# Performance work log

Measured on AMD Instinct MI355X. Metric: run time of the kernel, lower is better.

## Reference

```python
import jax, jax.numpy as jnp
import numpy as np

B, S, E = 2, 2048, 2048
H, KV, HD = 16, 4, 128  # num_heads, num_kv_heads, head_dim
G = H // KV             # query heads per kv head
ROPE_BASE = 10000.0


def rope_tables(dim, maxlen):
    freqs = 1.0 / ROPE_BASE ** (jnp.arange(0, dim, 2, dtype=jnp.float32) / dim)
    t = jnp.arange(maxlen, dtype=jnp.float32)
    f = jnp.outer(t, freqs)  # (maxlen, dim//2)
    return jnp.cos(f), jnp.sin(f)


def apply_rope(x, cos, sin):
    # x: (..., seq, heads, head_dim); interleaved-pair rotation
    s_len = x.shape[-3]
    c = cos[:s_len][:, None, :]
    s = sin[:s_len][:, None, :]
    x1 = x[..., ::2]
    x2 = x[..., 1::2]
    return jnp.stack([x1 * c - x2 * s, x1 * s + x2 * c], axis=-1).reshape(x.shape)


def setup_inputs() -> dict:
    key = jax.random.key(0)
    kx, kq, kk, kv, ko = jax.random.split(key, 5)
    x = jax.random.normal(kx, (B, S, E), dtype=jnp.float32)
    Wq = jax.random.normal(kq, (E, H * HD), dtype=jnp.float32) * 0.02
    Wk = jax.random.normal(kk, (E, KV * HD), dtype=jnp.float32) * 0.02
    Wv = jax.random.normal(kv, (E, KV * HD), dtype=jnp.float32) * 0.02
    Wo = jax.random.normal(ko, (H * HD, E), dtype=jnp.float32) * 0.02
    mask = jnp.tril(jnp.ones((S, S), dtype=bool))[None, None]  # causal (1,1,S,S)
    return {"x": x, "Wq": Wq, "Wk": Wk, "Wv": Wv, "Wo": Wo, "mask": mask}


def reference(x, Wq, Wk, Wv, Wo, mask):
    b, s, _ = x.shape
    cos, sin = rope_tables(HD, s)
    q = (x @ Wq).reshape(b, s, H, HD)
    k = (x @ Wk).reshape(b, s, KV, HD)
    v = (x @ Wv).reshape(b, s, KV, HD)
    q = apply_rope(q, cos, sin)
    k = apply_rope(k, cos, sin)
    if G > 1:
        k = jnp.repeat(k, G, axis=2)  # (b, s, H, HD)
        v = jnp.repeat(v, G, axis=2)
    q = jnp.transpose(q, (0, 2, 1, 3))  # (b, H, s, HD)
    k = jnp.transpose(k, (0, 2, 1, 3))
    v = jnp.transpose(v, (0, 2, 1, 3))
    scale = jnp.sqrt(jnp.float32(HD)).astype(q.dtype)
    scores = jnp.einsum("bhqd,bhkd->bhqk", q, k) / scale
    scores = jnp.where(mask, scores, jnp.finfo(scores.dtype).min)
    attn = jax.nn.softmax(scores, axis=-1)
    out = jnp.einsum("bhqk,bhkd->bhqd", attn, v)
    out = jnp.transpose(out, (0, 2, 1, 3)).reshape(b, s, H * HD)
    return out @ Wo
```

## Files before the change

kernel.cpp:

```cpp
#include <hip/hip_runtime.h>
#include <hip/hip_bf16.h>
#include <cstdint>

#define B_ 2
#define S_ 2048
#define E_ 2048
#define H_ 16
#define KV_ 4
#define HD_ 128
#define BS_ (B_*S_)
#define QKV_LD 3072
#define SM_SCALE 0.08838834764831845f
#define SC_LOG2E 0.1275424488538497f

typedef __attribute__((ext_vector_type(8))) __bf16 bf16x8;
typedef __attribute__((ext_vector_type(4))) float  floatx4;

__device__ __forceinline__ unsigned short f2bf(float f) {
  union { float f; unsigned u; } v; v.f = f;
  unsigned r = v.u + 0x7fffu + ((v.u >> 16) & 1u);
  return (unsigned short)(r >> 16);
}
__device__ __forceinline__ float bf2f(unsigned short u) {
  union { unsigned u; float f; } v; v.u = ((unsigned)u) << 16; return v.f;
}
__device__ __forceinline__ unsigned pack_bf16x2(float a, float b) {
  union { __hip_bfloat162 h; unsigned u; } v;
  v.h = __float22bfloat162_rn(make_float2(a, b));
  return v.u;
}

__device__ __forceinline__ void async_cp16(const void* g, void* l) {
  __builtin_amdgcn_global_load_lds(
      (const __attribute__((address_space(1))) void*)g,
      (__attribute__((address_space(3))) void*)l, 16, 0, 0);
}

__global__ __launch_bounds__(256)
void cvt_bf16(const float* __restrict__ src, unsigned short* __restrict__ dst,
              int n4) {
  int idx = blockIdx.x * 256 + threadIdx.x;
  if (idx >= n4) return;
  float4 v = *(const float4*)(src + (size_t)idx * 4);
  ushort4 o;
  o.x = f2bf(v.x); o.y = f2bf(v.y); o.z = f2bf(v.z); o.w = f2bf(v.w);
  *(ushort4*)(dst + (size_t)idx * 4) = o;
}

__global__ __launch_bounds__(256)
void cvt_bf16_t(const float* __restrict__ src, unsigned short* __restrict__ dst,
                int N, int dld, int noff) {
  __shared__ float tile[64 * 65];
  const int t = threadIdx.x;
  const int bk = blockIdx.y * 64, bn = blockIdx.x * 64;
  const int r = t >> 2, cg = t & 3;
#pragma unroll
  for (int i = 0; i < 4; ++i) {
    int c = cg * 16 + i * 4;
    float4 v = *(const float4*)(src + (size_t)(bk + r) * N + bn + c);
    tile[r * 65 + c] = v.x; tile[r * 65 + c + 1] = v.y;
    tile[r * 65 + c + 2] = v.z; tile[r * 65 + c + 3] = v.w;
  }
  __syncthreads();
  const int nl = t >> 2, kg = t & 3;
  union { unsigned short u[16]; uint4 q[2]; } o;
#pragma unroll
  for (int j = 0; j < 16; ++j)
    o.u[j] = f2bf(tile[(kg * 16 + j) * 65 + nl]);
  unsigned short* dp = dst + (size_t)(noff + bn + nl) * dld + bk + kg * 16;
  *(uint4*)(dp) = o.q[0];
  *(uint4*)(dp + 8) = o.q[1];
}

__global__ __launch_bounds__(256)
void rope_kernel(unsigned short* __restrict__ qkv) {
  const int PPR = 1280;
  int idx = blockIdx.x * 256 + threadIdx.x;
  if (idx >= BS_ * PPR) return;
  int row = idx / PPR, p = idx - row * PPR;
  int col = (p < 1024) ? (2 * p) : (2048 + 2 * (p - 1024));
  int d = p & 63;
  int s = row & (S_ - 1);
  float freq = expf(-(float)d * 0.14391156831212787f);
  float ang = (float)s * freq;
  float c = cosf(ang), sn = sinf(ang);
  unsigned short* ptr = qkv + (size_t)row * QKV_LD + col;
  float x1 = bf2f(ptr[0]), x2 = bf2f(ptr[1]);
  ptr[0] = f2bf(x1 * c - x2 * sn);
  ptr[1] = f2bf(x1 * sn + x2 * c);
}

__global__ __launch_bounds__(256)
void vtrans_kernel(const unsigned short* __restrict__ qkv,
                   unsigned short* __restrict__ vt) {
  __shared__ unsigned short tile[64 * 72];
  const int tid = threadIdx.x;
  const int s0 = blockIdx.x * 64;
  const int g = blockIdx.y >> 1;
  const int hh = (blockIdx.y & 1) * 64;
  const int b = g >> 2, kvh = g & 3;
#pragma unroll
  for (int i = 0; i < 2; ++i) {
    int chunk = tid + i * 256;
    int r = chunk >> 3, c = (chunk & 7) * 8;
    uint4 v = *(const uint4*)(qkv + (size_t)(b * S_ + s0 + r) * QKV_LD + 2560 + kvh * HD_ + hh + c);
    *(uint4*)(tile + r * 72 + c) = v;
  }
  __syncthreads();
#pragma unroll
  for (int i = 0; i < 2; ++i) {
    int chunk = tid + i * 256;
    int hdr = chunk >> 3, sc = (chunk & 7) * 8;
    union { unsigned short u[8]; uint4 v; } t;
#pragma unroll
    for (int j = 0; j < 8; ++j) t.u[j] = tile[(sc + j) * 72 + hdr];
    *(uint4*)(vt + (size_t)(g * HD_ + hh + hdr) * S_ + s0 + sc) = t.v;
  }
}

template<bool OUT_BF16>
__global__ __launch_bounds__(512, 2)
void gemm8(const unsigned short* __restrict__ A,
           const unsigned short* __restrict__ BT,
           void* __restrict__ C, int M, int N, int K) {
  __shared__ unsigned short Ash[2][256 * 64];
  __shared__ unsigned short Bsh[2][256 * 64];
  const int tid = threadIdx.x, l = tid & 63, w = tid >> 6;
  const int l16 = l & 15, l4 = l >> 4;
  const int w2 = w >> 2, w3 = w & 3;

  const int ntn = (int)gridDim.x;
  const int nwg = (int)(gridDim.x * gridDim.y);
  const int orig = (int)blockIdx.y * ntn + (int)blockIdx.x;
  const int cpx = nwg >> 3;
  const int swz = (orig & 7) * cpx + (orig >> 3);
  const int bm = (swz / ntn) * 256, bn = (swz % ntn) * 256;

  const int srow = tid >> 3;
  const int sgrp = ((tid & 7) - (tid >> 3)) & 7;
  const unsigned short* Asrc = A  + (size_t)(bm + srow) * K + sgrp * 8;
  const unsigned short* Bsrc = BT + (size_t)(bn + srow) * K + sgrp * 8;
  const int ldst = w * 512;

#define STAGE_A8(buf, H, kb) do { \
    async_cp16(Asrc + (size_t)((H) * 128) * K + (kb),      &Ash[buf][(H) * 8192 + ldst]); \
    async_cp16(Asrc + (size_t)((H) * 128 + 64) * K + (kb), &Ash[buf][(H) * 8192 + 4096 + ldst]); \
  } while (0)
#define STAGE_B8(buf, H, kb) do { \
    async_cp16(Bsrc + (size_t)((H) * 128) * K + (kb),      &Bsh[buf][(H) * 8192 + ldst]); \
    async_cp16(Bsrc + (size_t)((H) * 128 + 64) * K + (kb), &Bsh[buf][(H) * 8192 + 4096 + ldst]); \
  } while (0)
#define BAR8() __builtin_amdgcn_s_barrier()
#define VMCNT4() asm volatile("s_waitcnt vmcnt(4)" ::: "memory")

  const int s0 = ((l4 + l16) & 7) * 8;
  const int s1 = ((l4 + l16 + 4) & 7) * 8;
  const int arb = w2 * 64 + l16;
  const int brb = w3 * 32 + l16;

  const int nkt = K >> 6;

  STAGE_B8(0, 0, 0);
  STAGE_A8(0, 1, 0);
  STAGE_A8(0, 0, 0);
  STAGE_B8(0, 1, 0);
  {
    const int kb1 = (nkt > 1) ? 64 : 0;
    STAGE_B8(1, 0, kb1);
    STAGE_A8(1, 1, kb1);
  }
  VMCNT4(); BAR8();

  floatx4 acc[2][4][2][2] = {};

  for (int kt = 0; kt < nkt; ++kt) {
    const int cur = kt & 1;
    const int kb1 = ((kt + 1 < nkt) ? kt + 1 : nkt - 1) << 6;
    const int kb2 = ((kt + 2 < nkt) ? kt + 2 : nkt - 1) << 6;
    bf16x8 a[4][2], b0[2][2], b1[2][2];

#pragma unroll
    for (int m = 0; m < 4; ++m) {
      const int rA = 128 + arb + m * 16;
      a[m][0] = *(const bf16x8*)(&Ash[cur][rA * 64 + s0]);
      a[m][1] = *(const bf16x8*)(&Ash[cur][rA * 64 + s1]);
    }
#pragma unroll
    for (int n = 0; n < 2; ++n) {
      const int rB = brb + n * 16;
      b0[n][0] = *(const bf16x8*)(&Bsh[cur][rB * 64 + s0]);
      b0[n][1] = *(const bf16x8*)(&Bsh[cur][rB * 64 + s1]);
    }
    STAGE_A8(cur ^ 1, 0, kb1);
    BAR8();
    __builtin_amdgcn_s_setprio(1);
#pragma unroll
    for (int m = 0; m < 4; ++m)
#pragma unroll
      for (int n = 0; n < 2; ++n) {
        acc[1][m][0][n] = __builtin_amdgcn_mfma_f32_16x16x32_bf16(a[m][0], b0[n][0], acc[1][m][0][n], 0, 0, 0);
        acc[1][m][0][n] = __builtin_amdgcn_mfma_f32_16x16x32_bf16(a[m][1], b0[n][1], acc[1][m][0][n], 0, 0, 0);
      }
    __builtin_amdgcn_s_setprio(0);
    BAR8();

#pragma unroll
    for (int n = 0; n < 2; ++n) {
      const int rB = 128 + brb + n * 16;
      b1[n][0] = *(const bf16x8*)(&Bsh[cur][rB * 64 + s0]);
      b1[n][1] = *(const bf16x8*)(&Bsh[cur][rB * 64 + s1]);
    }
    STAGE_B8(cur ^ 1, 1, kb1);
    BAR8();
    __builtin_amdgcn_s_setprio(1);
#pragma unroll
    for (int m = 0; m < 4; ++m)
#pragma unroll
      for (int n = 0; n < 2; ++n) {
        acc[1][m][1][n] = __builtin_amdgcn_mfma_f32_16x16x32_bf16(a[m][0], b1[n][0], acc[1][m][1][n], 0, 0, 0);
        acc[1][m][1][n] = __builtin_amdgcn_mfma_f32_16x16x32_bf16(a[m][1], b1[n][1], acc[1][m][1][n], 0, 0, 0);
      }
    __builtin_amdgcn_s_setprio(0);
    BAR8();

#pragma unroll
    for (int m = 0; m < 4; ++m) {
      const int rA = arb + m * 16;
      a[m][0] = *(const bf16x8*)(&Ash[cur][rA * 64 + s0]);
      a[m][1] = *(const bf16x8*)(&Ash[cur][rA * 64 + s1]);
    }
    STAGE_B8(cur, 0, kb2);
    BAR8();
    __builtin_amdgcn_s_setprio(1);
#pragma unroll
    for (int m = 0; m < 4; ++m)
#pragma unroll
      for (int n = 0; n < 2; ++n) {
        acc[0][m][1][n] = __builtin_amdgcn_mfma_f32_16x16x32_bf16(a[m][0], b1[n][0], acc[0][m][1][n], 0, 0, 0);
        acc[0][m][1][n] = __builtin_amdgcn_mfma_f32_16x16x32_bf16(a[m][1], b1[n][1], acc[0][m][1][n], 0, 0, 0);
      }
    __builtin_amdgcn_s_setprio(0);
    BAR8();

    STAGE_A8(cur, 1, kb2);
    BAR8();
    __builtin_amdgcn_s_setprio(1);
#pragma unroll
    for (int m = 0; m < 4; ++m)
#pragma unroll
      for (int n = 0; n < 2; ++n) {
        acc[0][m][0][n] = __builtin_amdgcn_mfma_f32_16x16x32_bf16(a[m][0], b0[n][0], acc[0][m][0][n], 0, 0, 0);
        acc[0][m][0][n] = __builtin_amdgcn_mfma_f32_16x16x32_bf16(a[m][1], b0[n][1], acc[0][m][0][n], 0, 0, 0);
      }
    __builtin_amdgcn_s_setprio(0);
    VMCNT4();
    BAR8();
  }

  asm volatile("s_waitcnt vmcnt(0)" ::: "memory");

#pragma unroll
  for (int mh = 0; mh < 2; ++mh)
#pragma unroll
    for (int m = 0; m < 4; ++m)
#pragma unroll
      for (int nh = 0; nh < 2; ++nh)
#pragma unroll
        for (int n = 0; n < 2; ++n) {
          const int row0 = bm + mh * 128 + w2 * 64 + m * 16 + l4 * 4;
          const int col  = bn + nh * 128 + w3 * 32 + n * 16 + l16;
#pragma unroll
          for (int rr = 0; rr < 4; ++rr) {
            float v = acc[mh][m][nh][n][rr];
            if (OUT_BF16) ((unsigned short*)C)[(size_t)(row0 + rr) * N + col] = f2bf(v);
            else          ((float*)C)[(size_t)(row0 + rr) * N + col] = v;
          }
        }
#undef STAGE_A8
#undef STAGE_B8
#undef BAR8
#undef VMCNT4
}

__global__ __launch_bounds__(512, 2)
void gqa_attention(const unsigned short* __restrict__ qkv,
                   const unsigned short* __restrict__ vt,
                   unsigned short* __restrict__ out) {
  __shared__ unsigned short Ksh[2][2][32 * 128];
  __shared__ unsigned short Vsh[2][2][128 * 32];

  const int tid = threadIdx.x, l = tid & 63, wave = tid >> 6;
  const int l16 = l & 15, l4 = l >> 4;
  const int hw = wave & 3, seg = wave >> 2;
  const int g = blockIdx.x, b = g >> 2, kvh = g & 3;
  const int h = kvh * 4 + hw;
  const int y = blockIdx.y;

  const int k_subrow = l >> 4;
  const int v_subrow = l >> 2;
  const int gv = (((l & 3) - (l >> 4)) & 3) * 8;

  const unsigned short* kp[2];
  const unsigned short* vp[2];
#pragma unroll
  for (int i = 0; i < 2; ++i) {
    int cc = hw + i * 4;
    int krow = 4 * cc + k_subrow;
    int gk = (((l & 15) - krow) & 15) * 8;
    kp[i] = qkv + (size_t)(b * S_ + krow) * QKV_LD + 2048 + kvh * HD_ + gk;
    vp[i] = vt + (size_t)(g * HD_ + 16 * cc + v_subrow) * S_ + gv;
  }

  for (int phase = 0; phase < 2; ++phase) {
    const int t = phase ? (63 - y) : y;
    const int qt = t * 32;
    const int nch = t + 1;
    const int c0 = nch >> 1;
    const int st = nch - c0;

    bf16x8 qfA[4], qfB[4];
    {
      const unsigned short* qpA = qkv + (size_t)(b * S_ + qt + l16) * QKV_LD + h * HD_;
      const unsigned short* qpB = qpA + (size_t)16 * QKV_LD;
#pragma unroll
      for (int c = 0; c < 4; ++c) {
        qfA[c] = *(const bf16x8*)(qpA + c * 32 + l4 * 8);
        qfB[c] = *(const bf16x8*)(qpB + c * 32 + l4 * 8);
      }
    }
    asm volatile("s_waitcnt vmcnt(0)" ::: "memory");
    asm volatile("s_barrier" ::: "memory");

    {
      const int ci = (seg == 0) ? 0 : c0;
      const int ko = ci * 32 * QKV_LD, vo = ci * 32;
#pragma unroll
      for (int i = 0; i < 2; ++i) {
        int cc = hw + i * 4;
        async_cp16(kp[i] + ko, &Ksh[seg][0][cc * 512]);
        async_cp16(vp[i] + vo, &Vsh[seg][0][cc * 512]);
      }
    }

    float lsumA = 0.f, lsumB = 0.f;
    floatx4 accA[8] = {}, accB[8] = {};

    for (int step = 0; step < st; ++step) {
      const int cur = step & 1;
      asm volatile("s_barrier" ::: "memory");
      {
        const int cn = step + 1;
        const int cnext = (seg == 0) ? ((cn < c0) ? cn : 0)
                                     : ((cn < st) ? (c0 + cn) : 0);
        const int ko = cnext * 32 * QKV_LD, vo = cnext * 32;
#pragma unroll
        for (int i = 0; i < 2; ++i) {
          int cc = hw + i * 4;
          async_cp16(kp[i] + ko, &Ksh[seg][cur ^ 1][cc * 512]);
          async_cp16(vp[i] + vo, &Vsh[seg][cur ^ 1][cc * 512]);
        }
      }
      asm volatile("s_waitcnt vmcnt(4)\n\ts_barrier" ::: "memory");

      const bool active = (seg == 1) || (step < c0);
      if (active) {
        const bool tri = (seg == 1) && (step == st - 1);

        floatx4 sA[2] = {}, sB[2] = {};
#pragma unroll
        for (int half = 0; half < 2; ++half) {
          const int krow = half * 16 + l16;
#pragma unroll
          for (int c = 0; c < 4; ++c) {
            const int s = (c * 4 + l4 + l16) & 15;
            bf16x8 kf = *(const bf16x8*)(&Ksh[seg][cur][krow * 128 + s * 8]);
            sA[half] = __builtin_amdgcn_mfma_f32_16x16x32_bf16(kf, qfA[c], sA[half], 0, 0, 0);
            sB[half] = __builtin_amdgcn_mfma_f32_16x16x32_bf16(kf, qfB[c], sB[half], 0, 0, 0);
          }
        }

        float pA[8], pB[8];
#pragma unroll
        for (int half = 0; half < 2; ++half)
#pragma unroll
          for (int r = 0; r < 4; ++r) {
            float vA = fminf(sA[half][r] * SC_LOG2E, 80.f);
            float vB = fminf(sB[half][r] * SC_LOG2E, 80.f);
            if (tri) {
              int kk = half * 16 + l4 * 4 + r;
              if (kk > l16) vA = -3e38f;
              if (half == 1 && (l4 * 4 + r) > l16) vB = -3e38f;
            }
            float eA = exp2f(vA), eB = exp2f(vB);
            pA[half * 4 + r] = eA; lsumA += eA;
            pB[half * 4 + r] = eB; lsumB += eB;
          }

        unsigned a0 = pack_bf16x2(pA[0], pA[1]);
        unsigned a1 = pack_bf16x2(pA[2], pA[3]);
        unsigned a2 = pack_bf16x2(pA[4], pA[5]);
        unsigned a3 = pack_bf16x2(pA[6], pA[7]);
        asm("v_permlane32_swap_b32 %0, %1" : "+v"(a0), "+v"(a2));
        asm("v_permlane16_swap_b32 %0, %1" : "+v"(a0), "+v"(a2));
        asm("v_permlane32_swap_b32 %0, %1" : "+v"(a1), "+v"(a3));
        asm("v_permlane16_swap_b32 %0, %1" : "+v"(a1), "+v"(a3));
        unsigned b0 = pack_bf16x2(pB[0], pB[1]);
        unsigned b1 = pack_bf16x2(pB[2], pB[3]);
        unsigned b2 = pack_bf16x2(pB[4], pB[5]);
        unsigned b3 = pack_bf16x2(pB[6], pB[7]);
        asm("v_permlane32_swap_b32 %0, %1" : "+v"(b0), "+v"(b2));
        asm("v_permlane16_swap_b32 %0, %1" : "+v"(b0), "+v"(b2));
        asm("v_permlane32_swap_b32 %0, %1" : "+v"(b1), "+v"(b3));
        asm("v_permlane16_swap_b32 %0, %1" : "+v"(b1), "+v"(b3));
        union { unsigned w[4]; bf16x8 v8; } punA, punB;
        punA.w[0] = a0; punA.w[1] = a1; punA.w[2] = a2; punA.w[3] = a3;
        punB.w[0] = b0; punB.w[1] = b1; punB.w[2] = b2; punB.w[3] = b3;
        const bf16x8 pfA = punA.v8;
        const bf16x8 pfB = punB.v8;

#pragma unroll
        for (int u = 0; u < 8; ++u) {
          const int row = u * 16 + l16;
          const int s = (l4 + (l16 >> 2)) & 3;
          bf16x8 vf = *(const bf16x8*)(&Vsh[seg][cur][row * 32 + s * 8]);
          accA[u] = __builtin_amdgcn_mfma_f32_16x16x32_bf16(vf, pfA, accA[u], 0, 0, 0);
          accB[u] = __builtin_amdgcn_mfma_f32_16x16x32_bf16(vf, pfB, accB[u], 0, 0, 0);
        }
      }
    }

    asm volatile("s_waitcnt vmcnt(0)" ::: "memory");
    __syncthreads();
    float* combA = (float*)(&Ksh[0][0][0]);
    float* combL = (float*)(&Vsh[0][0][0]);
    if (seg == 1) {
#pragma unroll
      for (int u = 0; u < 8; ++u)
        *(floatx4*)(combA + ((hw * 8 + u) * 64 + l) * 4) = accA[u];
      combL[(hw * 64 + l) * 2]     = lsumA;
      combL[(hw * 64 + l) * 2 + 1] = lsumB;
    }
    __syncthreads();
    if (seg == 0) {
#pragma unroll
      for (int u = 0; u < 8; ++u)
        accA[u] += *(const floatx4*)(combA + ((hw * 8 + u) * 64 + l) * 4);
      lsumA += combL[(hw * 64 + l) * 2];
      lsumB += combL[(hw * 64 + l) * 2 + 1];
    }
    __syncthreads();
    if (seg == 1) {
#pragma unroll
      for (int u = 0; u < 8; ++u)
        *(floatx4*)(combA + ((hw * 8 + u) * 64 + l) * 4) = accB[u];
    }
    __syncthreads();
    if (seg == 0) {
#pragma unroll
      for (int u = 0; u < 8; ++u)
        accB[u] += *(const floatx4*)(combA + ((hw * 8 + u) * 64 + l) * 4);

      lsumA += __shfl_xor(lsumA, 16, 64);
      lsumA += __shfl_xor(lsumA, 32, 64);
      lsumB += __shfl_xor(lsumB, 16, 64);
      lsumB += __shfl_xor(lsumB, 32, 64);
      float invA = 1.0f / lsumA;
      float invB = 1.0f / lsumB;
      unsigned short* opA = out + (size_t)(b * S_ + qt + l16) * 2048 + h * HD_;
      unsigned short* opB = opA + (size_t)16 * 2048;
#pragma unroll
      for (int u = 0; u < 8; ++u) {
        uint2 oA, oB;
        oA.x = pack_bf16x2(accA[u][0] * invA, accA[u][1] * invA);
        oA.y = pack_bf16x2(accA[u][2] * invA, accA[u][3] * invA);
        *(uint2*)(opA + u * 16 + l4 * 4) = oA;
        oB.x = pack_bf16x2(accB[u][0] * invB, accB[u][1] * invB);
        oB.y = pack_bf16x2(accB[u][2] * invB, accB[u][3] * invB);
        *(uint2*)(opB + u * 16 + l4 * 4) = oB;
      }
    }
  }
}

extern "C" void kernel_launch(void* const* d_in, const int* in_sizes, int n_in,
                              void* d_out, int out_size, void* d_ws, size_t ws_size,
                              hipStream_t stream) {
  const float* x  = (const float*)d_in[0];
  const float* Wq = (const float*)d_in[1];
  const float* Wk = (const float*)d_in[2];
  const float* Wv = (const float*)d_in[3];
  const float* Wo = (const float*)d_in[4];
  float* out = (float*)d_out;

  char* ws = (char*)d_ws;
  unsigned short* xb    = (unsigned short*)(ws);
  unsigned short* wqkvT = (unsigned short*)(ws + 16777216);
  unsigned short* woT   = (unsigned short*)(ws + 29360128);
  unsigned short* qkv   = (unsigned short*)(ws + 37748736);
  unsigned short* attn  = (unsigned short*)(ws + 62914560);
  unsigned short* vt    = (unsigned short*)(ws);

  cvt_bf16<<<(4096 * 2048 / 4 + 255) / 256, 256, 0, stream>>>(x, xb, 4096 * 2048 / 4);
  cvt_bf16_t<<<dim3(32, 32), 256, 0, stream>>>(Wq, wqkvT, 2048, 2048, 0);
  cvt_bf16_t<<<dim3(8, 32),  256, 0, stream>>>(Wk, wqkvT, 512,  2048, 2048);
  cvt_bf16_t<<<dim3(8, 32),  256, 0, stream>>>(Wv, wqkvT, 512,  2048, 2560);
  cvt_bf16_t<<<dim3(32, 32), 256, 0, stream>>>(Wo, woT,  2048, 2048, 0);

  gemm8<true><<<dim3(12, 16), 512, 0, stream>>>(xb, wqkvT, qkv, 4096, 3072, 2048);
  rope_kernel<<<(4096 * 1280 + 255) / 256, 256, 0, stream>>>(qkv);
  vtrans_kernel<<<dim3(32, 16), 256, 0, stream>>>(qkv, vt);
  gqa_attention<<<dim3(8, 32), 512, 0, stream>>>(qkv, vt, attn);
  gemm8<false><<<dim3(8, 16), 512, 0, stream>>>(attn, woT, out, 4096, 2048, 2048);
}
```

Baseline: 359.1 us.

## Fuse RoPE into QKV GEMM epilogue, restage prefetch, use simple GEMM for output

Removes the standalone RoPE kernel and applies the rotation inside the QKV GEMM epilogue, using a lane shuffle to fetch each pair partner, which saves a full read-modify-write pass over Q and K. The GEMM prefetch schedule is reordered so that all loads for tile kt+2 are issued within iteration kt, with a deeper vmcnt wait and one fewer barrier. The output projection switches from the tuned 256x256 gemm8 to a new simple 128x128 single-buffered gemm_tn kernel, which may be slower because it does not overlap loads with compute.

```diff
diff --git a/kernel.cpp b/kernel.cpp
--- a/kernel.cpp
+++ b/kernel.cpp
@@ -73,24 +73,6 @@
 }
 
 __global__ __launch_bounds__(256)
-void rope_kernel(unsigned short* __restrict__ qkv) {
-  const int PPR = 1280;
-  int idx = blockIdx.x * 256 + threadIdx.x;
-  if (idx >= BS_ * PPR) return;
-  int row = idx / PPR, p = idx - row * PPR;
-  int col = (p < 1024) ? (2 * p) : (2048 + 2 * (p - 1024));
-  int d = p & 63;
-  int s = row & (S_ - 1);
-  float freq = expf(-(float)d * 0.14391156831212787f);
-  float ang = (float)s * freq;
-  float c = cosf(ang), sn = sinf(ang);
-  unsigned short* ptr = qkv + (size_t)row * QKV_LD + col;
-  float x1 = bf2f(ptr[0]), x2 = bf2f(ptr[1]);
-  ptr[0] = f2bf(x1 * c - x2 * sn);
-  ptr[1] = f2bf(x1 * sn + x2 * c);
-}
-
-__global__ __launch_bounds__(256)
 void vtrans_kernel(const unsigned short* __restrict__ qkv,
                    unsigned short* __restrict__ vt) {
   __shared__ unsigned short tile[64 * 72];
@@ -119,10 +101,70 @@
 }
 
 template<bool OUT_BF16>
+__global__ __launch_bounds__(256, 2)
+void gemm_tn(const unsigned short* __restrict__ A,
+             const unsigned short* __restrict__ BT,
+             void* __restrict__ C, int M, int N, int K) {
+  __shared__ unsigned short Ash[128 * 32];
+  __shared__ unsigned short Bsh[128 * 32];
+  const int tid = threadIdx.x;
+  const int l = tid & 63;
+  const int l16 = l & 15, l4 = l >> 4;
+  const int wave = tid >> 6;
+  const int wm = (wave >> 1) * 64, wn = (wave & 1) * 64;
+  const int bm = blockIdx.y * 128, bn = blockIdx.x * 128;
+
+  const int srow = l >> 2;
+  const int sg = (((l & 3) - (l >> 4)) & 3) * 8;
+
+  floatx4 acc[4][4] = {};
+
+  for (int kb = 0; kb < K; kb += 32) {
+    __syncthreads();
+#pragma unroll
+    for (int i = 0; i < 2; ++i) {
+      int cc = wave + i * 4;
+      async_cp16(A + (size_t)(bm + 16 * cc + srow) * K + kb + sg, &Ash[cc * 512]);
+      async_cp16(BT + (size_t)(bn + 16 * cc + srow) * K + kb + sg, &Bsh[cc * 512]);
+    }
+    __syncthreads();
+    bf16x8 af[4], bf[4];
+#pragma unroll
+    for (int t = 0; t < 4; ++t) {
+      int row = wm + t * 16 + l16;
+      int s = (l4 + (l16 >> 2)) & 3;
+      af[t] = *(const bf16x8*)(Ash + row * 32 + s * 8);
+    }
+#pragma unroll
+    for (int t = 0; t < 4; ++t) {
+      int row = wn + t * 16 + l16;
+      int s = (l4 + (l16 >> 2)) & 3;
+      bf[t] = *(const bf16x8*)(Bsh + row * 32 + s * 8);
+    }
+#pragma unroll
+    for (int tm = 0; tm < 4; ++tm)
+#pragma unroll
+      for (int tn = 0; tn < 4; ++tn)
+        acc[tm][tn] = __builtin_amdgcn_mfma_f32_16x16x32_bf16(af[tm], bf[tn], acc[tm][tn], 0, 0, 0);
+  }
+#pragma unroll
+  for (int tm = 0; tm < 4; ++tm)
+#pragma unroll
+    for (int tn = 0; tn < 4; ++tn)
+#pragma unroll
+      for (int r = 0; r < 4; ++r) {
+        int row = bm + wm + tm * 16 + l4 * 4 + r;
+        int col = bn + wn + tn * 16 + l16;
+        float v = acc[tm][tn][r];
+        if (OUT_BF16) ((unsigned short*)C)[(size_t)row * N + col] = f2bf(v);
+        else          ((float*)C)[(size_t)row * N + col] = v;
+      }
+}
+
 __global__ __launch_bounds__(512, 2)
-void gemm8(const unsigned short* __restrict__ A,
-           const unsigned short* __restrict__ BT,
-           void* __restrict__ C, int M, int N, int K) {
+void gemm8_rope(const unsigned short* __restrict__ A,
+                const unsigned short* __restrict__ BT,
+                unsigned short* __restrict__ C, int M, int N, int K) {
   __shared__ unsigned short Ash[2][256 * 64];
   __shared__ unsigned short Bsh[2][256 * 64];
   const int tid = threadIdx.x, l = tid & 63, w = tid >> 6;
@@ -142,16 +184,15 @@
   const unsigned short* Bsrc = BT + (size_t)(bn + srow) * K + sgrp * 8;
   const int ldst = w * 512;
 
-#define STAGE_A8(buf, H, kb) do { \
-    async_cp16(Asrc + (size_t)((H) * 128) * K + (kb),      &Ash[buf][(H) * 8192 + ldst]); \
-    async_cp16(Asrc + (size_t)((H) * 128 + 64) * K + (kb), &Ash[buf][(H) * 8192 + 4096 + ldst]); \
+#define STAGE_A8(buf, HH, kb) do { \
+    async_cp16(Asrc + (size_t)((HH) * 128) * K + (kb),      &Ash[buf][(HH) * 8192 + ldst]); \
+    async_cp16(Asrc + (size_t)((HH) * 128 + 64) * K + (kb), &Ash[buf][(HH) * 8192 + 4096 + ldst]); \
   } while (0)
-#define STAGE_B8(buf, H, kb) do { \
-    async_cp16(Bsrc + (size_t)((H) * 128) * K + (kb),      &Bsh[buf][(H) * 8192 + ldst]); \
-    async_cp16(Bsrc + (size_t)((H) * 128 + 64) * K + (kb), &Bsh[buf][(H) * 8192 + 4096 + ldst]); \
+#define STAGE_B8(buf, HH, kb) do { \
+    async_cp16(Bsrc + (size_t)((HH) * 128) * K + (kb),      &Bsh[buf][(HH) * 8192 + ldst]); \
+    async_cp16(Bsrc + (size_t)((HH) * 128 + 64) * K + (kb), &Bsh[buf][(HH) * 8192 + 4096 + ldst]); \
   } while (0)
 #define BAR8() __builtin_amdgcn_s_barrier()
-#define VMCNT4() asm volatile("s_waitcnt vmcnt(4)" ::: "memory")
 
   const int s0 = ((l4 + l16) & 7) * 8;
   const int s1 = ((l4 + l16 + 4) & 7) * 8;
@@ -160,22 +201,15 @@
 
   const int nkt = K >> 6;
 
-  STAGE_B8(0, 0, 0);
-  STAGE_A8(0, 1, 0);
-  STAGE_A8(0, 0, 0);
-  STAGE_B8(0, 1, 0);
-  {
-    const int kb1 = (nkt > 1) ? 64 : 0;
-    STAGE_B8(1, 0, kb1);
-    STAGE_A8(1, 1, kb1);
-  }
-  VMCNT4(); BAR8();
+  STAGE_A8(0, 1, 0); STAGE_B8(0, 0, 0); STAGE_B8(0, 1, 0); STAGE_A8(0, 0, 0);
+  STAGE_A8(1, 1, 64); STAGE_B8(1, 0, 64); STAGE_B8(1, 1, 64); STAGE_A8(1, 0, 64);
+  asm volatile("s_waitcnt vmcnt(8)" ::: "memory");
+  BAR8();
 
   floatx4 acc[2][4][2][2] = {};
 
   for (int kt = 0; kt < nkt; ++kt) {
     const int cur = kt & 1;
-    const int kb1 = ((kt + 1 < nkt) ? kt + 1 : nkt - 1) << 6;
     const int kb2 = ((kt + 2 < nkt) ? kt + 2 : nkt - 1) << 6;
     bf16x8 a[4][2], b0[2][2], b1[2][2];
 
@@ -191,7 +225,6 @@
       b0[n][0] = *(const bf16x8*)(&Bsh[cur][rB * 64 + s0]);
       b0[n][1] = *(const bf16x8*)(&Bsh[cur][rB * 64 + s1]);
     }
-    STAGE_A8(cur ^ 1, 0, kb1);
     BAR8();
     __builtin_amdgcn_s_setprio(1);
 #pragma unroll
@@ -210,7 +243,8 @@
       b1[n][0] = *(const bf16x8*)(&Bsh[cur][rB * 64 + s0]);
       b1[n][1] = *(const bf16x8*)(&Bsh[cur][rB * 64 + s1]);
     }
-    STAGE_B8(cur ^ 1, 1, kb1);
+    STAGE_A8(cur, 1, kb2);
+    STAGE_B8(cur, 0, kb2);
     BAR8();
     __builtin_amdgcn_s_setprio(1);
 #pragma unroll
@@ -229,7 +263,7 @@
       a[m][0] = *(const bf16x8*)(&Ash[cur][rA * 64 + s0]);
       a[m][1] = *(const bf16x8*)(&Ash[cur][rA * 64 + s1]);
     }
-    STAGE_B8(cur, 0, kb2);
+    STAGE_B8(cur, 1, kb2);
     BAR8();
     __builtin_amdgcn_s_setprio(1);
 #pragma unroll
@@ -242,8 +276,7 @@
     __builtin_amdgcn_s_setprio(0);
     BAR8();
 
-    STAGE_A8(cur, 1, kb2);
-    BAR8();
+    STAGE_A8(cur, 0, kb2);
     __builtin_amdgcn_s_setprio(1);
 #pragma unroll
     for (int m = 0; m < 4; ++m)
@@ -253,7 +286,7 @@
         acc[0][m][0][n] = __builtin_amdgcn_mfma_f32_16x16x32_bf16(a[m][1], b0[n][1], acc[0][m][0][n], 0, 0, 0);
       }
     __builtin_amdgcn_s_setprio(0);
-    VMCNT4();
+    asm volatile("s_waitcnt vmcnt(8)" ::: "memory");
     BAR8();
   }
 
@@ -269,17 +302,26 @@
         for (int n = 0; n < 2; ++n) {
           const int row0 = bm + mh * 128 + w2 * 64 + m * 16 + l4 * 4;
           const int col  = bn + nh * 128 + w3 * 32 + n * 16 + l16;
-#pragma unroll
-          for (int rr = 0; rr < 4; ++rr) {
-            float v = acc[mh][m][nh][n][rr];
-            if (OUT_BF16) ((unsigned short*)C)[(size_t)(row0 + rr) * N + col] = f2bf(v);
-            else          ((float*)C)[(size_t)(row0 + rr) * N + col] = v;
+          if (col < 2560) {
+            const int d = (col & 127) >> 1;
+            const float freq = expf(-(float)d * 0.14391156831212787f);
+            const float sgn = (l & 1) ? 1.f : -1.f;
+#pragma unroll
+            for (int rr = 0; rr < 4; ++rr) {
+              float own = acc[mh][m][nh][n][rr];
+              float part = __shfl_xor(own, 1, 64);
+              float ang = (float)((row0 + rr) & (S_ - 1)) * freq;
+              float cth = cosf(ang), sth = sinf(ang);
+              acc[mh][m][nh][n][rr] = own * cth + part * sth * sgn;
+            }
           }
+#pragma unroll
+          for (int rr = 0; rr < 4; ++rr)
+            C[(size_t)(row0 + rr) * N + col] = f2bf(acc[mh][m][nh][n][rr]);
         }
 #undef STAGE_A8
 #undef STAGE_B8
 #undef BAR8
-#undef VMCNT4
 }
 
 __global__ __launch_bounds__(512, 2)
@@ -506,9 +548,8 @@
   cvt_bf16_t<<<dim3(8, 32),  256, 0, stream>>>(Wv, wqkvT, 512,  2048, 2560);
   cvt_bf16_t<<<dim3(32, 32), 256, 0, stream>>>(Wo, woT,  2048, 2048, 0);
 
-  gemm8<true><<<dim3(12, 16), 512, 0, stream>>>(xb, wqkvT, qkv, 4096, 3072, 2048);
-  rope_kernel<<<(4096 * 1280 + 255) / 256, 256, 0, stream>>>(qkv);
+  gemm8_rope<<<dim3(12, 16), 512, 0, stream>>>(xb, wqkvT, qkv, 4096, 3072, 2048);
   vtrans_kernel<<<dim3(32, 16), 256, 0, stream>>>(qkv, vt);
   gqa_attention<<<dim3(8, 32), 512, 0, stream>>>(qkv, vt, attn);
-  gemm8<false><<<dim3(8, 16), 512, 0, stream>>>(attn, woT, out, 4096, 2048, 2048);
-}
+  gemm_tn<false><<<dim3(16, 32), 256, 0, stream>>>(attn, woT, out, 4096, 2048, 2048);
+}
```

Measured after the change: 382.0 us. 6.4% more time.
